# Performance work log

Measured on AMD Instinct MI355X. Metric: run time of the kernel, lower is better.

Reference implementation:

```python
import jax, jax.numpy as jnp
import numpy as np

N, E, F, H, R, NB, G, C = 100000, 500000, 128, 64, 16, 30, 1000, 10


def setup_inputs() -> dict:
    key = jax.random.key(0)
    ks = jax.random.split(key, 12)
    s = 0.05
    x = jax.random.normal(ks[0], (N, F), jnp.float32)
    edge_index = jax.random.randint(ks[1], (2, E), 0, N, dtype=jnp.int32)
    edge_norm = jax.random.uniform(ks[2], (E,), jnp.float32)
    edge_type = jax.random.randint(ks[3], (E,), 0, R, dtype=jnp.int32)
    seq_lengths = jnp.full((G,), N // G, dtype=jnp.int32)  # 1000 graphs x 100 nodes
    return dict(
        x=x, edge_index=edge_index, edge_norm=edge_norm, edge_type=edge_type,
        seq_lengths=seq_lengths, avec=0,
        w1_rel=jax.random.normal(ks[4], (F, H), jnp.float32) * s,
        w1_root=jax.random.normal(ks[5], (F, H), jnp.float32) * s,
        b1=jnp.zeros((H,), jnp.float32),
        bases=jax.random.normal(ks[6], (NB, H, H), jnp.float32) * s,
        comp=jax.random.normal(ks[7], (R, NB), jnp.float32) * s,
        w2_root=jax.random.normal(ks[8], (H, H), jnp.float32) * s,
        b2=jnp.zeros((H,), jnp.float32),
        lin_w=jax.random.normal(ks[9], (2 * (F + H), H), jnp.float32) * s,
        lin_b=jnp.zeros((H,), jnp.float32),
        fc_w=jax.random.normal(ks[10], (H, C), jnp.float32) * s,
        fc_b=jnp.zeros((C,), jnp.float32),
    )


def reference(x, edge_index, edge_norm, edge_type, seq_lengths, avec,
              w1_rel, w1_root, b1, bases, comp, w2_root, b2,
              lin_w, lin_b, fc_w, fc_b):
    src, dst = edge_index[0], edge_index[1]

    # --- GraphConv (PyG): out_i = W_rel @ sum_{j->i} w_ji x_j + W_root x_i + b
    msg = x[src] * edge_norm[:, None]                       # [E, F]
    agg = jax.ops.segment_sum(msg, dst, num_segments=N)     # [N, F]
    h = agg @ w1_rel + x @ w1_root + b1                     # [N, H]

    # --- RGCNConv with basis decomposition, mean aggregation per relation
    W = jnp.einsum('rb,bio->rio', comp, bases)              # [R, H, H]
    hs = h[src]                                             # [E, H]
    out = h @ w2_root + b2                                  # root transform + bias
    for r in range(R):  # small fixed relation count
        m = (edge_type == r).astype(h.dtype)                # [E]
        s_r = jax.ops.segment_sum(hs * m[:, None], dst, num_segments=N)
        c_r = jax.ops.segment_sum(m, dst, num_segments=N)
        out = out + (s_r / jnp.maximum(c_r, 1.0)[:, None]) @ W[r]

    feats = jnp.concatenate([x, out], axis=-1)              # [N, F+H]

    # --- ragged per-graph sum & max pooling (replaces the Python loop)
    bounds = jnp.cumsum(seq_lengths)
    gid = jnp.searchsorted(bounds, jnp.arange(N), side='right')  # [N] graph ids
    gsum = jax.ops.segment_sum(feats, gid, num_segments=G)       # [G, F+H]
    gmax = jax.ops.segment_max(feats, gid, num_segments=G)       # [G, F+H]

    hidden = jax.nn.relu(jnp.concatenate([gsum, gmax], -1) @ lin_w + lin_b)
    # dropout is identity at inference
    logits = hidden @ fc_w + fc_b                           # [G, C]
    if avec:
        return logits
    return jax.nn.log_softmax(logits, -1)
```

## Files before the change

kernel.cpp:

```cpp
#include <hip/hip_runtime.h>
#include <hip/hip_bf16.h>

#define NN 100000
#define NE 500000
#define FD 128
#define HD 64
#define RR 16
#define NBASE 30
#define GG 1000
#define CC 10
#define NGROUP 6250
#define NBLK ((NE + 255) / 256)
#define NDBLK ((NN + 256) / 256)
#define NOBLK (NN / 16)
#define TOTZ (NN * RR)
#define ZBLK ((TOTZ + 1023) / 1024)


typedef __attribute__((ext_vector_type(8))) short bf16x8;
typedef __attribute__((ext_vector_type(4))) float f32x4;

__device__ inline unsigned short f2b(float x) {
  __hip_bfloat16 b = __float2bfloat16(x);
  return *reinterpret_cast<unsigned short*>(&b);
}
__device__ inline float b2f(unsigned short u) {
  return __uint_as_float(((unsigned)u) << 16);
}
__device__ inline unsigned pk2(float a, float b) {
  return (unsigned)f2b(a) | ((unsigned)f2b(b) << 16);
}

__global__ void k_prep(const float* comp, const float* bases, const float* w_root,
                       const float* w_rel, const float* w2, unsigned short* Wt,
                       unsigned short* wcat2, unsigned short* w2t, int* zbase) {
  int bx = blockIdx.x;
  if (bx < 256) {
    int idx = bx * 256 + threadIdx.x;
    int r = idx >> 12, kj = idx & 4095;
    int k = kj >> 6, n = kj & 63;
    float acc = 0.0f;
    for (int b = 0; b < NBASE; ++b)
      acc += comp[r * NBASE + b] * bases[b * 4096 + kj];
    int sk = (k & 15) * 4 + (k >> 4);
    Wt[(r << 12) + n * 64 + sk] = f2b(acc);
  } else if (bx < 336) {
    int idx = (bx - 256) * 256 + threadIdx.x;
    if (idx < 16384) {
      int n = idx >> 7, k = idx & 127;
      float v = (n < 64) ? w_root[k * 64 + n] : w_rel[k * 64 + (n - 64)];
      int nt = n >> 4, m = n & 15;
      int s = k >> 5, q = (k >> 3) & 3, j = k & 7;
      wcat2[(((nt * 4 + s) * 64) + q * 16 + m) * 8 + j] = f2b(v);
    } else if (idx < 16384 + 4096) {
      int i2 = idx - 16384;
      int n = i2 >> 6, k = i2 & 63;
      int sk = (k & 15) * 4 + (k >> 4);
      w2t[n * 64 + sk] = f2b(w2[k * 64 + n]);
    }
  } else {
    int idx = (bx - 336) * 1024 + threadIdx.x * 4;
    if (idx < TOTZ)
      *reinterpret_cast<int4*>(zbase + idx) = make_int4(0, 0, 0, 0);
  }
}

__global__ __launch_bounds__(256) void k_proj_mfma(const float* x, const unsigned short* wcat2,
                                                   const float* b1, unsigned short* hroot_bf,
                                                   unsigned short* xw_bf) {
  __shared__ unsigned short wsh[16384];
  int wv = threadIdx.x >> 6, l = threadIdx.x & 63, m = l & 15, q = l >> 4;
  int g = blockIdx.x * 4 + wv;
  int gc = (g < NGROUP) ? g : (NGROUP - 1);
  size_t n0 = (size_t)gc * 16;
  const float* xr = x + (n0 + m) * FD + q * 8;
  float4 xv[8];
#pragma unroll
  for (int s = 0; s < 4; ++s) {
    xv[2 * s] = *reinterpret_cast<const float4*>(xr + s * 32);
    xv[2 * s + 1] = *reinterpret_cast<const float4*>(xr + s * 32 + 4);
  }
  {
    const uint4* wsrc = reinterpret_cast<const uint4*>(wcat2);
    uint4* wdst = reinterpret_cast<uint4*>(wsh);
#pragma unroll
    for (int r = 0; r < 8; ++r)
      wdst[r * 256 + threadIdx.x] = wsrc[r * 256 + threadIdx.x];
  }
  __syncthreads();
  if (g >= NGROUP) return;
  bf16x8 afr[4];
#pragma unroll
  for (int s = 0; s < 4; ++s) {
    float4 xa = xv[2 * s], xb = xv[2 * s + 1];
    bf16x8 a;
    a[0] = (short)f2b(xa.x); a[1] = (short)f2b(xa.y);
    a[2] = (short)f2b(xa.z); a[3] = (short)f2b(xa.w);
    a[4] = (short)f2b(xb.x); a[5] = (short)f2b(xb.y);
    a[6] = (short)f2b(xb.z); a[7] = (short)f2b(xb.w);
    afr[s] = a;
  }
  f32x4 acc[8];
#pragma unroll
  for (int nt = 0; nt < 8; ++nt) acc[nt] = (f32x4){0, 0, 0, 0};
#pragma unroll
  for (int s = 0; s < 4; ++s) {
#pragma unroll
    for (int nt = 0; nt < 8; ++nt) {
      bf16x8 b = *reinterpret_cast<const bf16x8*>(wsh + (size_t)((nt * 4 + s) * 64 + l) * 8);
      acc[nt] = __builtin_amdgcn_mfma_f32_16x16x32_bf16(afr[s], b, acc[nt], 0, 0, 0);
    }
  }
  float bv[4];
#pragma unroll
  for (int nt = 0; nt < 4; ++nt) bv[nt] = b1[nt * 16 + m];
#pragma unroll
  for (int i = 0; i < 4; ++i) {
    size_t row = (n0 + q * 4 + i) * 64 + m * 4;
    uint2 oh, ox;
    oh.x = pk2(acc[0][i] + bv[0], acc[1][i] + bv[1]);
    oh.y = pk2(acc[2][i] + bv[2], acc[3][i] + bv[3]);
    ox.x = pk2(acc[4][i], acc[5][i]);
    ox.y = pk2(acc[6][i], acc[7][i]);
    *reinterpret_cast<uint2*>(hroot_bf + row) = oh;
    *reinterpret_cast<uint2*>(xw_bf + row) = ox;
  }
}

__global__ void k_hists(const int* ei, const int* etype, int* bch, int* hist2) {
  __shared__ int lh[RR];
  if (threadIdx.x < RR) lh[threadIdx.x] = 0;
  __syncthreads();
  int e = blockIdx.x * 256 + threadIdx.x;
  if (e < NE) {
    int t = etype[e];
    atomicAdd(&lh[t], 1);
    atomicAdd(&hist2[ei[NE + e] * RR + t], 1);
  }
  __syncthreads();
  if (threadIdx.x < RR) bch[blockIdx.x * RR + threadIdx.x] = lh[threadIdx.x];
}

__device__ inline int block_scan_incl(int v, int* ps, int t) {
  ps[t] = v;
  __syncthreads();
  for (int off = 1; off < 256; off <<= 1) {
    int u = (t >= off) ? ps[t - off] : 0;
    __syncthreads();
    ps[t] += u;
    __syncthreads();
  }
  return ps[t];
}

__device__ inline int dst_degree(const int* hist2, int dst) {
  const int4* hp = reinterpret_cast<const int4*>(hist2 + dst * RR);
  int4 a = hp[0], b = hp[1], c = hp[2], d = hp[3];
  return a.x + a.y + a.z + a.w + b.x + b.y + b.z + b.w +
         c.x + c.y + c.z + c.w + d.x + d.y + d.z + d.w;
}

__global__ void k_scanA(const int* hist2, int* bsum) {
  __shared__ int red[256];
  int t = threadIdx.x;
  int dst = blockIdx.x * 256 + t;
  red[t] = (dst < NN) ? dst_degree(hist2, dst) : 0;
  __syncthreads();
  for (int s = 128; s; s >>= 1) {
    if (t < s) red[t] += red[t + s];
    __syncthreads();
  }
  if (t == 0) bsum[blockIdx.x] = red[0];
}

__global__ void k_scanC(const int* hist2, const int* bsum, int* rowptr_d, int* ctr_d) {
  int t = threadIdx.x;
  int dst = blockIdx.x * 256 + t;
  int v = (dst < NN) ? dst_degree(hist2, dst) : 0;
  __shared__ int ps[256];
  int incl = block_scan_incl(v, ps, t);
  int ex = bsum[blockIdx.x] + incl - v;
  if (dst <= NN) { rowptr_d[dst] = ex; ctr_d[dst] = ex; }
}

__global__ void k_bscan(const int* bch, const int* seq, int* bsum, int* bbase,
                        int* offs, int* bounds) {
  __shared__ int part[16][17], chunkbase[16][17];
  __shared__ int colbase[16];
  __shared__ int ps[256];
  int t = threadIdx.x;
  {
    int i0 = t * 2, i1 = t * 2 + 1;
    int l0 = (i0 < NDBLK) ? bsum[i0] : 0;
    int l1 = (i1 < NDBLK) ? bsum[i1] : 0;
    int sa = l0 + l1;
    int incla = block_scan_incl(sa, ps, t);
    int run = incla - sa;
    if (i0 < NDBLK) bsum[i0] = run;
    run += l0;
    if (i1 < NDBLK) bsum[i1] = run;
  }
  __syncthreads();
  int ty = t & 15, ck = t >> 4;
  const int CH = (NBLK + 15) / 16;
  int b0 = ck * CH, b1 = min(b0 + CH, NBLK);
  int s = 0;
  for (int b = b0; b < b1; ++b) s += bch[b * 16 + ty];
  part[ck][ty] = s;
  __syncthreads();
  if (t < 16) {
    int run = 0;
    for (int c = 0; c < 16; ++c) { chunkbase[c][t] = run; run += part[c][t]; }
    colbase[t] = run;
  }
  __syncthreads();
  if (t == 0) {
    int run = 0;
    for (int r = 0; r < RR; ++r) { int v = colbase[r]; offs[r] = run; colbase[r] = run; run += v; }
    offs[RR] = run;
  }
  __syncthreads();
  {
    int run = colbase[ty] + chunkbase[ck][ty];
    for (int b = b0; b < b1; ++b) {
      int v = bch[b * 16 + ty];
      bbase[b * 16 + ty] = run;
      run += v;
    }
  }
  __syncthreads();
  int loc[4];
  int ss = 0;
  if (t < 250) {
    for (int i = 0; i < 4; ++i) { loc[i] = seq[t * 4 + i]; ss += loc[i]; }
  }
  int incl = block_scan_incl(ss, ps, t);
  int base = incl - ss;
  if (t < 250) {
    int run = base;
    for (int i = 0; i < 4; ++i) { run += loc[i]; bounds[t * 4 + i] = run; }
  }
}

__global__ void k_sort(const int* ei, const int* etype, const float* enorm,
                       const int* bbase, const int* hist2, int* ctr_d,
                       uint4* tse, uint2* esen) {
  __shared__ int lcnt[RR];
  if (threadIdx.x < RR) lcnt[threadIdx.x] = 0;
  __syncthreads();
  int e = blockIdx.x * 256 + threadIdx.x;
  if (e >= NE) return;
  int t = etype[e];
  int rank = atomicAdd(&lcnt[t], 1);
  int p = bbase[blockIdx.x * RR + t] + rank;
  int src = ei[e];
  int dst = ei[NE + e];
  int cnt = hist2[dst * RR + t];
  float inv = 1.0f / (float)max(cnt, 1);
  int pos = atomicAdd(&ctr_d[dst], 1);
  esen[pos] = make_uint2((unsigned)src, __float_as_uint(enorm[e]));
  tse[p] = make_uint4((unsigned)src, __float_as_uint(inv), (unsigned)pos, 0u);
}

__global__ __launch_bounds__(256) void k_gconv_seg(const int* rowptr_d, const uint2* esen,
    const unsigned short* xw_bf, const unsigned short* hroot_bf, unsigned short* h_bf) {
  int wv = threadIdx.x >> 6, l = threadIdx.x & 63;
  int c4 = l & 15, eq = l >> 4;
  int dst = blockIdx.x * 4 + wv;
  int lo = rowptr_d[dst];
  int hi = rowptr_d[dst + 1];
  float4 acc = {0.0f, 0.0f, 0.0f, 0.0f};
  for (int base0 = lo; base0 < hi; base0 += 64) {
    int n = min(64, hi - base0);
    int sv = 0;
    float nv = 0.0f;
    if (l < n) {
      uint2 se = esen[base0 + l];
      sv = (int)se.x;
      nv = __uint_as_float(se.y);
    }
    int k4max = (n + 3) >> 2;
    for (int k4 = 0; k4 < k4max; ++k4) {
      int eid = k4 * 4 + eq;
      int s = __shfl(sv, eid);
      float w = __shfl(nv, eid);
      if (eid < n) {
        uint2 v = *reinterpret_cast<const uint2*>(xw_bf + (size_t)s * 64 + c4 * 4);
        acc.x += b2f((unsigned short)(v.x & 0xffffu)) * w;
        acc.y += b2f((unsigned short)(v.x >> 16)) * w;
        acc.z += b2f((unsigned short)(v.y & 0xffffu)) * w;
        acc.w += b2f((unsigned short)(v.y >> 16)) * w;
      }
    }
  }
  acc.x += __shfl_xor(acc.x, 16); acc.y += __shfl_xor(acc.y, 16);
  acc.z += __shfl_xor(acc.z, 16); acc.w += __shfl_xor(acc.w, 16);
  acc.x += __shfl_xor(acc.x, 32); acc.y += __shfl_xor(acc.y, 32);
  acc.z += __shfl_xor(acc.z, 32); acc.w += __shfl_xor(acc.w, 32);
  if (l < 16) {
    uint2 hb = *reinterpret_cast<const uint2*>(hroot_bf + (size_t)dst * 64 + l * 4);
    acc.x += b2f((unsigned short)(hb.x & 0xffffu));
    acc.y += b2f((unsigned short)(hb.x >> 16));
    acc.z += b2f((unsigned short)(hb.y & 0xffffu));
    acc.w += b2f((unsigned short)(hb.y >> 16));
    uint2 o;
    o.x = pk2(acc.x, acc.y);
    o.y = pk2(acc.z, acc.w);
    *reinterpret_cast<uint2*>(h_bf + (size_t)dst * 64 + l * 4) = o;
  }
}

__global__ __launch_bounds__(256) void k_rgcn_y(const uint4* tse, const int* offs,
    const unsigned short* h_bf, const unsigned short* Wt, unsigned short* y_bf) {
  int r = blockIdx.x;
  int lo = offs[r], hi = offs[r + 1];
  int cnt = hi - lo;
  int wv = threadIdx.x >> 6;
  int l = threadIdx.x & 63;
  int m = l & 15, q = l >> 4;
  int ngroups = (cnt + 15) / 16;
  const unsigned short* Wr = Wt + (r << 12);
  bf16x8 bfr[2][4];
#pragma unroll
  for (int s = 0; s < 2; ++s)
#pragma unroll
    for (int nt = 0; nt < 4; ++nt)
      bfr[s][nt] = *reinterpret_cast<const bf16x8*>(Wr + (nt * 16 + m) * 64 + s * 32 + q * 8);

  for (int g = blockIdx.y * 4 + wv; g < ngroups; g += gridDim.y * 4) {
    int base = lo + g * 16;
    int ne = min(16, hi - base);
    int p = base + ((m < ne) ? m : 0);
    uint4 t4 = tse[p];
    int src = (int)t4.x;
    float inv = __uint_as_float(t4.y);
    int pos = (int)t4.z;
    f32x4 acc[4];
#pragma unroll
    for (int nt = 0; nt < 4; ++nt) acc[nt] = (f32x4){0, 0, 0, 0};
    const unsigned short* hrow = h_bf + (size_t)src * 64 + q * 8;
#pragma unroll
    for (int s = 0; s < 2; ++s) {
      bf16x8 afr = *reinterpret_cast<const bf16x8*>(hrow + s * 32);
#pragma unroll
      for (int nt = 0; nt < 4; ++nt)
        acc[nt] = __builtin_amdgcn_mfma_f32_16x16x32_bf16(afr, bfr[s][nt], acc[nt], 0, 0, 0);
    }
#pragma unroll
    for (int i = 0; i < 4; ++i) {
      int row = q * 4 + i;
      float ir = __shfl(inv, row);
      int pr = __shfl(pos, row);
      if (row < ne) {
        uint2 o;
        o.x = pk2(acc[0][i] * ir, acc[1][i] * ir);
        o.y = pk2(acc[2][i] * ir, acc[3][i] * ir);
        *reinterpret_cast<uint2*>(y_bf + (size_t)pr * 64 + m * 4) = o;
      }
    }
  }
}

__global__ __launch_bounds__(256) void k_out(const int* rowptr_d, const unsigned short* y_bf,
    const unsigned short* h_bf, const unsigned short* w2t, const float* b2,
    const int* bounds, float* psum_p, float* pmax_p) {
  __shared__ float ldsC[16][68];
  __shared__ int gidv[16];
  int wv = threadIdx.x >> 6, l = threadIdx.x & 63;
  int c8 = l & 7, eq8 = l >> 3;
  size_t d0 = (size_t)blockIdx.x * 16;
  if (threadIdx.x < 16) {
    int dst = (int)d0 + threadIdx.x;
    int lo2 = 0, hi2 = GG;
    while (lo2 < hi2) {
      int mid = (lo2 + hi2) >> 1;
      if (bounds[mid] <= dst) lo2 = mid + 1; else hi2 = mid;
    }
    gidv[threadIdx.x] = lo2;
  }
  for (int dd = 0; dd < 4; ++dd) {
    int dst = (int)d0 + wv * 4 + dd;
    int lo = rowptr_d[dst];
    int hi = rowptr_d[dst + 1];
    float4 aA = {0.0f, 0.0f, 0.0f, 0.0f};
    float4 aB = {0.0f, 0.0f, 0.0f, 0.0f};
    for (int row = lo + eq8; row < hi; row += 8) {
      uint4 v = *reinterpret_cast<const uint4*>(y_bf + (size_t)row * 64 + c8 * 8);
      aA.x += b2f((unsigned short)(v.x & 0xffffu));
      aA.y += b2f((unsigned short)(v.x >> 16));
      aA.z += b2f((unsigned short)(v.y & 0xffffu));
      aA.w += b2f((unsigned short)(v.y >> 16));
      aB.x += b2f((unsigned short)(v.z & 0xffffu));
      aB.y += b2f((unsigned short)(v.z >> 16));
      aB.z += b2f((unsigned short)(v.w & 0xffffu));
      aB.w += b2f((unsigned short)(v.w >> 16));
    }
#pragma unroll
    for (int off = 8; off <= 32; off <<= 1) {
      aA.x += __shfl_xor(aA.x, off); aA.y += __shfl_xor(aA.y, off);
      aA.z += __shfl_xor(aA.z, off); aA.w += __shfl_xor(aA.w, off);
      aB.x += __shfl_xor(aB.x, off); aB.y += __shfl_xor(aB.y, off);
      aB.z += __shfl_xor(aB.z, off); aB.w += __shfl_xor(aB.w, off);
    }
    if (l < 8) {
      *reinterpret_cast<float4*>(&ldsC[wv * 4 + dd][l * 8]) = aA;
      *reinterpret_cast<float4*>(&ldsC[wv * 4 + dd][l * 8 + 4]) = aB;
    }
  }
  __syncthreads();
  int m = l & 15, q = l >> 4, nt = wv;
  float bb = b2[nt * 16 + m];
  f32x4 acc;
#pragma unroll
  for (int i = 0; i < 4; ++i) acc[i] = ldsC[q * 4 + i][m * 4 + nt] + bb;
#pragma unroll
  for (int s = 0; s < 2; ++s) {
    bf16x8 a = *reinterpret_cast<const bf16x8*>(h_bf + (d0 + m) * 64 + s * 32 + q * 8);
    bf16x8 b = *reinterpret_cast<const bf16x8*>(w2t + (nt * 16 + m) * 64 + s * 32 + q * 8);
    acc = __builtin_amdgcn_mfma_f32_16x16x32_bf16(a, b, acc, 0, 0, 0);
  }
  int c = nt * 16 + m;
  int gA = gidv[0];
  float sA = 0.0f, xA = -3.4e38f, sB = 0.0f, xB = -3.4e38f;
#pragma unroll
  for (int i = 0; i < 4; ++i) {
    int gi = gidv[q * 4 + i];
    if (gi == gA) { sA += acc[i]; xA = fmaxf(xA, acc[i]); }
    else          { sB += acc[i]; xB = fmaxf(xB, acc[i]); }
  }
#pragma unroll
  for (int off = 16; off <= 32; off <<= 1) {
    sA += __shfl_xor(sA, off); xA = fmaxf(xA, __shfl_xor(xA, off));
    sB += __shfl_xor(sB, off); xB = fmaxf(xB, __shfl_xor(xB, off));
  }
  if (q == 0) {
    size_t base = (size_t)blockIdx.x * 128;
    psum_p[base + c] = sA;
    psum_p[base + 64 + c] = sB;
    pmax_p[base + c] = xA;
    pmax_p[base + 64 + c] = xB;
  }
}

__global__ __launch_bounds__(256) void k_head(const float* x, const int* bounds,
    const float* psum_p, const float* pmax_p, const float* lin_w, const float* lin_b,
    const float* fc_w, const float* fc_b, float* dout) {
  __shared__ float4 psum[8][32], pmax[8][32];
  __shared__ float gsum[192], gmax[192];
  __shared__ float part[4][64];
  __shared__ float hid[HD], lg[CC], mred[2];
  int g = blockIdx.x, t = threadIdx.x;
  int lo = (g == 0) ? 0 : bounds[g - 1];
  int hi = bounds[g];
  int nn = hi - lo;
  {
    int c4 = t & 31, ch = t >> 5;
    int a = lo + (nn * ch) / 8, b = lo + (nn * (ch + 1)) / 8;
    float4 s = {0, 0, 0, 0};
    float4 mx = {-3.4e38f, -3.4e38f, -3.4e38f, -3.4e38f};
    const float* bp = x + (size_t)a * FD + c4 * 4;
    int n = a;
    for (; n + 4 <= b; n += 4) {
      float4 v0 = *reinterpret_cast<const float4*>(bp);
      float4 v1 = *reinterpret_cast<const float4*>(bp + FD);
      float4 v2 = *reinterpret_cast<const float4*>(bp + 2 * FD);
      float4 v3 = *reinterpret_cast<const float4*>(bp + 3 * FD);
      bp += 4 * FD;
      s.x += v0.x + v1.x + v2.x + v3.x;
      s.y += v0.y + v1.y + v2.y + v3.y;
      s.z += v0.z + v1.z + v2.z + v3.z;
      s.w += v0.w + v1.w + v2.w + v3.w;
      mx.x = fmaxf(fmaxf(fmaxf(mx.x, v0.x), fmaxf(v1.x, v2.x)), v3.x);
      mx.y = fmaxf(fmaxf(fmaxf(mx.y, v0.y), fmaxf(v1.y, v2.y)), v3.y);
      mx.z = fmaxf(fmaxf(fmaxf(mx.z, v0.z), fmaxf(v1.z, v2.z)), v3.z);
      mx.w = fmaxf(fmaxf(fmaxf(mx.w, v0.w), fmaxf(v1.w, v2.w)), v3.w);
    }
    for (; n < b; ++n) {
      float4 v = *reinterpret_cast<const float4*>(bp);
      bp += FD;
      s.x += v.x; s.y += v.y; s.z += v.z; s.w += v.w;
      mx.x = fmaxf(mx.x, v.x); mx.y = fmaxf(mx.y, v.y);
      mx.z = fmaxf(mx.z, v.z); mx.w = fmaxf(mx.w, v.w);
    }
    psum[ch][c4] = s;
    pmax[ch][c4] = mx;
  }
  __syncthreads();
  if (t < 32) {
    float4 s = psum[0][t], m = pmax[0][t];
#pragma unroll
    for (int ch = 1; ch < 8; ++ch) {
      float4 ps = psum[ch][t], pm = pmax[ch][t];
      s.x += ps.x; s.y += ps.y; s.z += ps.z; s.w += ps.w;
      m.x = fmaxf(m.x, pm.x); m.y = fmaxf(m.y, pm.y);
      m.z = fmaxf(m.z, pm.z); m.w = fmaxf(m.w, pm.w);
    }
    gsum[t * 4 + 0] = s.x; gsum[t * 4 + 1] = s.y;
    gsum[t * 4 + 2] = s.z; gsum[t * 4 + 3] = s.w;
    gmax[t * 4 + 0] = m.x; gmax[t * 4 + 1] = m.y;
    gmax[t * 4 + 2] = m.z; gmax[t * 4 + 3] = m.w;
  } else if (t < 96) {
    int c = t - 32;
    int blo = lo >> 4, bhi = (hi - 1) >> 4;
    float s = 0.0f, mx = -3.4e38f;
    for (int b = blo; b <= bhi; ++b) {
      size_t base = (size_t)b * 128;
      if (b * 16 >= lo) {
        s += psum_p[base + c];
        mx = fmaxf(mx, pmax_p[base + c]);
      }
      if (b * 16 + 15 < hi) {
        s += psum_p[base + 64 + c];
        mx = fmaxf(mx, pmax_p[base + 64 + c]);
      }
    }
    gsum[128 + c] = s;
    gmax[128 + c] = mx;
  }
  __syncthreads();
  {
    int o = t & 63, pp = t >> 6;
    float a = 0.0f;
    int k0 = pp * 96;
    for (int k = k0; k < k0 + 96; ++k) {
      float gv = (k < 192) ? gsum[k] : gmax[k - 192];
      a += gv * lin_w[k * 64 + o];
    }
    part[pp][o] = a;
  }
  __syncthreads();
  if (t < HD) {
    float a = lin_b[t] + part[0][t] + part[1][t] + part[2][t] + part[3][t];
    hid[t] = fmaxf(a, 0.0f);
  }
  __syncthreads();
  if (t < CC) {
    float a = fc_b[t];
    for (int k = 0; k < HD; ++k) a += hid[k] * fc_w[k * CC + t];
    lg[t] = a;
  }
  __syncthreads();
  if (t == 0) {
    float mm = lg[0];
#pragma unroll
    for (int i = 1; i < CC; ++i) mm = fmaxf(mm, lg[i]);
    float se = 0.0f;
#pragma unroll
    for (int i = 0; i < CC; ++i) se += __expf(lg[i] - mm);
    mred[0] = mm;
    mred[1] = __logf(se);
  }
  __syncthreads();
  if (t < CC) dout[g * CC + t] = lg[t] - mred[0] - mred[1];
}

extern "C" void kernel_launch(void* const* d_in, const int* in_sizes, int n_in,
                              void* d_out, int out_size, void* d_ws, size_t ws_size,
                              hipStream_t stream) {
  const float* x     = (const float*)d_in[0];
  const int* ei      = (const int*)d_in[1];
  const float* enorm = (const float*)d_in[2];
  const int* etype   = (const int*)d_in[3];
  const int* seq     = (const int*)d_in[4];
  const float* w1_rel  = (const float*)d_in[6];
  const float* w1_root = (const float*)d_in[7];
  const float* b1      = (const float*)d_in[8];
  const float* bases   = (const float*)d_in[9];
  const float* comp    = (const float*)d_in[10];
  const float* w2      = (const float*)d_in[11];
  const float* b2      = (const float*)d_in[12];
  const float* lin_w   = (const float*)d_in[13];
  const float* lin_b   = (const float*)d_in[14];
  const float* fc_w    = (const float*)d_in[15];
  const float* fc_b    = (const float*)d_in[16];
  float* dout = (float*)d_out;

  char* p = (char*)d_ws;
  unsigned short* hroot_bf = (unsigned short*)p; p += (size_t)NN * 64 * 2;
  unsigned short* xw_bf    = (unsigned short*)p; p += (size_t)NN * 64 * 2;
  unsigned short* y_bf = (unsigned short*)p; p += (size_t)NE * 64 * 2;
  unsigned short* h_bf = (unsigned short*)p; p += (size_t)NN * 64 * 2;
  unsigned short* Wt   = (unsigned short*)p; p += (size_t)RR * 4096 * 2;
  unsigned short* wcat2 = (unsigned short*)p; p += (size_t)128 * 128 * 2;
  unsigned short* w2t  = (unsigned short*)p; p += (size_t)64 * 64 * 2;
  uint4* tse   = (uint4*)p; p += (size_t)NE * 16;
  uint2* esen  = (uint2*)p; p += (size_t)NE * 8;
  int* hist2   = (int*)p; p += (size_t)NN * RR * 4;
  float* psum_p = (float*)p; p += (size_t)NOBLK * 128 * 4;
  float* pmax_p = (float*)p; p += (size_t)NOBLK * 128 * 4;
  int* rowptr_d = (int*)p; p += (size_t)(NDBLK * 256) * 4;
  int* ctr_d   = (int*)p; p += (size_t)(NDBLK * 256) * 4;
  int* bch     = (int*)p; p += (size_t)NBLK * RR * 4;
  int* bbase   = (int*)p; p += (size_t)NBLK * RR * 4;
  int* bsum    = (int*)p; p += (size_t)NGROUP * 4;
  int* offs    = (int*)p; p += 68;
  int* bounds  = (int*)p; p += (size_t)GG * 4;

  hipLaunchKernelGGL(k_prep, dim3(336 + ZBLK), dim3(256), 0, stream,
                     comp, bases, w1_root, w1_rel, w2, Wt, wcat2, w2t, hist2);
  hipLaunchKernelGGL(k_proj_mfma, dim3((NGROUP + 3) / 4), dim3(256), 0, stream,
                     x, wcat2, b1, hroot_bf, xw_bf);
  hipLaunchKernelGGL(k_hists, dim3(NBLK), dim3(256), 0, stream, ei, etype, bch, hist2);
  hipLaunchKernelGGL(k_scanA, dim3(NDBLK), dim3(256), 0, stream, hist2, bsum);
  hipLaunchKernelGGL(k_bscan, dim3(1), dim3(256), 0, stream, bch, seq, bsum, bbase, offs, bounds);
  hipLaunchKernelGGL(k_scanC, dim3(NDBLK), dim3(256), 0, stream, hist2, bsum, rowptr_d, ctr_d);
  hipLaunchKernelGGL(k_sort, dim3(NBLK), dim3(256), 0, stream,
                     ei, etype, enorm, bbase, hist2, ctr_d, tse, esen);
  hipLaunchKernelGGL(k_gconv_seg, dim3(NN / 4), dim3(256), 0, stream,
                     rowptr_d, esen, xw_bf, hroot_bf, h_bf);
  hipLaunchKernelGGL(k_rgcn_y, dim3(RR, 128), dim3(256), 0, stream,
                     tse, offs, h_bf, Wt, y_bf);
  hipLaunchKernelGGL(k_out, dim3(NOBLK), dim3(256), 0, stream,
                     rowptr_d, y_bf, h_bf, w2t, b2, bounds, psum_p, pmax_p);
  hipLaunchKernelGGL(k_head, dim3(GG), dim3(256), 0, stream, x, bounds,
                     psum_p, pmax_p, lin_w, lin_b, fc_w, fc_b, dout);
}
```

Before: 338.4 us.

## Fuse x pooling partials into projection kernel and narrow k_out gather lanes

```diff
diff --git a/kernel.cpp b/kernel.cpp
--- a/kernel.cpp
+++ b/kernel.cpp
@@ -13,6 +13,7 @@
 #define NBLK ((NE + 255) / 256)
 #define NDBLK ((NN + 256) / 256)
 #define NOBLK (NN / 16)
+#define NPBLK ((NGROUP + 3) / 4)
 #define TOTZ (NN * RR)
 #define ZBLK ((TOTZ + 1023) / 1024)
 
@@ -31,9 +32,22 @@
   return (unsigned)f2b(a) | ((unsigned)f2b(b) << 16);
 }
 
+__device__ inline int block_scan_incl(int v, int* ps, int t) {
+  ps[t] = v;
+  __syncthreads();
+  for (int off = 1; off < 256; off <<= 1) {
+    int u = (t >= off) ? ps[t - off] : 0;
+    __syncthreads();
+    ps[t] += u;
+    __syncthreads();
+  }
+  return ps[t];
+}
+
 __global__ void k_prep(const float* comp, const float* bases, const float* w_root,
-                       const float* w_rel, const float* w2, unsigned short* Wt,
-                       unsigned short* wcat2, unsigned short* w2t, int* zbase) {
+                       const float* w_rel, const float* w2, const int* seq,
+                       unsigned short* Wt, unsigned short* wcat2, unsigned short* w2t,
+                       int* zbase, int* bounds) {
   int bx = blockIdx.x;
   if (bx < 256) {
     int idx = bx * 256 + threadIdx.x;
@@ -58,20 +72,38 @@
       int sk = (k & 15) * 4 + (k >> 4);
       w2t[n * 64 + sk] = f2b(w2[k * 64 + n]);
     }
+  } else if (bx == 336) {
+    __shared__ int ps[256];
+    int t = threadIdx.x;
+    int loc[4];
+    int ss = 0;
+    if (t < 250) {
+      for (int i = 0; i < 4; ++i) { loc[i] = seq[t * 4 + i]; ss += loc[i]; }
+    }
+    int incl = block_scan_incl(ss, ps, t);
+    int base = incl - ss;
+    if (t < 250) {
+      int run = base;
+      for (int i = 0; i < 4; ++i) { run += loc[i]; bounds[t * 4 + i] = run; }
+    }
   } else {
-    int idx = (bx - 336) * 1024 + threadIdx.x * 4;
+    int idx = (bx - 337) * 1024 + threadIdx.x * 4;
     if (idx < TOTZ)
       *reinterpret_cast<int4*>(zbase + idx) = make_int4(0, 0, 0, 0);
   }
 }
 
 __global__ __launch_bounds__(256) void k_proj_mfma(const float* x, const unsigned short* wcat2,
-                                                   const float* b1, unsigned short* hroot_bf,
-                                                   unsigned short* xw_bf) {
+                                                   const float* b1, const int* bounds,
+                                                   unsigned short* hroot_bf, unsigned short* xw_bf,
+                                                   float* pxsum, float* pxmax) {
   __shared__ unsigned short wsh[16384];
+  __shared__ float pxs[4][2][128], pxm[4][2][128];
+  __shared__ int binfo;
   int wv = threadIdx.x >> 6, l = threadIdx.x & 63, m = l & 15, q = l >> 4;
   int g = blockIdx.x * 4 + wv;
-  int gc = (g < NGROUP) ? g : (NGROUP - 1);
+  bool active = (g < NGROUP);
+  int gc = active ? g : (NGROUP - 1);
   size_t n0 = (size_t)gc * 16;
   const float* xr = x + (n0 + m) * FD + q * 8;
   float4 xv[8];
@@ -87,8 +119,17 @@
     for (int r = 0; r < 8; ++r)
       wdst[r * 256 + threadIdx.x] = wsrc[r * 256 + threadIdx.x];
   }
-  __syncthreads();
-  if (g >= NGROUP) return;
+  if (threadIdx.x == 0) {
+    int n0b = blockIdx.x * 64;
+    int lo2 = 0, hi2 = GG;
+    while (lo2 < hi2) {
+      int mid = (lo2 + hi2) >> 1;
+      if (bounds[mid] <= n0b) lo2 = mid + 1; else hi2 = mid;
+    }
+    binfo = bounds[lo2];
+  }
+  __syncthreads();
+  int bnd = binfo;
   bf16x8 afr[4];
 #pragma unroll
   for (int s = 0; s < 4; ++s) {
@@ -111,19 +152,67 @@
       acc[nt] = __builtin_amdgcn_mfma_f32_16x16x32_bf16(afr[s], b, acc[nt], 0, 0, 0);
     }
   }
-  float bv[4];
-#pragma unroll
-  for (int nt = 0; nt < 4; ++nt) bv[nt] = b1[nt * 16 + m];
-#pragma unroll
-  for (int i = 0; i < 4; ++i) {
-    size_t row = (n0 + q * 4 + i) * 64 + m * 4;
-    uint2 oh, ox;
-    oh.x = pk2(acc[0][i] + bv[0], acc[1][i] + bv[1]);
-    oh.y = pk2(acc[2][i] + bv[2], acc[3][i] + bv[3]);
-    ox.x = pk2(acc[4][i], acc[5][i]);
-    ox.y = pk2(acc[6][i], acc[7][i]);
-    *reinterpret_cast<uint2*>(hroot_bf + row) = oh;
-    *reinterpret_cast<uint2*>(xw_bf + row) = ox;
+  if (active) {
+    float bv[4];
+#pragma unroll
+    for (int nt = 0; nt < 4; ++nt) bv[nt] = b1[nt * 16 + m];
+#pragma unroll
+    for (int i = 0; i < 4; ++i) {
+      size_t row = (n0 + q * 4 + i) * 64 + m * 4;
+      uint2 oh, ox;
+      oh.x = pk2(acc[0][i] + bv[0], acc[1][i] + bv[1]);
+      oh.y = pk2(acc[2][i] + bv[2], acc[3][i] + bv[3]);
+      ox.x = pk2(acc[4][i], acc[5][i]);
+      ox.y = pk2(acc[6][i], acc[7][i]);
+      *reinterpret_cast<uint2*>(hroot_bf + row) = oh;
+      *reinterpret_cast<uint2*>(xw_bf + row) = ox;
+    }
+  }
+  {
+    int row = (int)n0 + m;
+    bool inA = active && (row < bnd);
+    bool inB = active && (row >= bnd);
+#pragma unroll
+    for (int s = 0; s < 4; ++s) {
+      float v[8] = { xv[2 * s].x, xv[2 * s].y, xv[2 * s].z, xv[2 * s].w,
+                     xv[2 * s + 1].x, xv[2 * s + 1].y, xv[2 * s + 1].z, xv[2 * s + 1].w };
+#pragma unroll
+      for (int sl = 0; sl < 2; ++sl) {
+        bool in = sl ? inB : inA;
+        float sv[8], mv[8];
+#pragma unroll
+        for (int j = 0; j < 8; ++j) {
+          sv[j] = in ? v[j] : 0.0f;
+          mv[j] = in ? v[j] : -3.4e38f;
+        }
+#pragma unroll
+        for (int off = 1; off <= 8; off <<= 1) {
+#pragma unroll
+          for (int j = 0; j < 8; ++j) {
+            sv[j] += __shfl_xor(sv[j], off);
+            mv[j] = fmaxf(mv[j], __shfl_xor(mv[j], off));
+          }
+        }
+        if (m == 0) {
+#pragma unroll
+          for (int j = 0; j < 8; ++j) {
+            pxs[wv][sl][s * 32 + q * 8 + j] = sv[j];
+            pxm[wv][sl][s * 32 + q * 8 + j] = mv[j];
+          }
+        }
+      }
+    }
+  }
+  __syncthreads();
+  {
+    int t = threadIdx.x;
+    int sl = t >> 7, c = t & 127;
+    float s4 = pxs[0][sl][c] + pxs[1][sl][c] + pxs[2][sl][c] + pxs[3][sl][c];
+    float m4 = fmaxf(fmaxf(pxm[0][sl][c], pxm[1][sl][c]),
+                     fmaxf(pxm[2][sl][c], pxm[3][sl][c]));
+    size_t base = (size_t)blockIdx.x * 256 + sl * 128 + c;
+    pxsum[base] = s4;
+    pxmax[base] = m4;
   }
 }
 
@@ -139,18 +228,6 @@
   }
   __syncthreads();
   if (threadIdx.x < RR) bch[blockIdx.x * RR + threadIdx.x] = lh[threadIdx.x];
-}
-
-__device__ inline int block_scan_incl(int v, int* ps, int t) {
-  ps[t] = v;
-  __syncthreads();
-  for (int off = 1; off < 256; off <<= 1) {
-    int u = (t >= off) ? ps[t - off] : 0;
-    __syncthreads();
-    ps[t] += u;
-    __syncthreads();
-  }
-  return ps[t];
 }
 
 __device__ inline int dst_degree(const int* hist2, int dst) {
@@ -183,8 +260,7 @@
   if (dst <= NN) { rowptr_d[dst] = ex; ctr_d[dst] = ex; }
 }
 
-__global__ void k_bscan(const int* bch, const int* seq, int* bsum, int* bbase,
-                        int* offs, int* bounds) {
+__global__ void k_bscan(const int* bch, int* bsum, int* bbase, int* offs) {
   __shared__ int part[16][17], chunkbase[16][17];
   __shared__ int colbase[16];
   __shared__ int ps[256];
@@ -227,18 +303,6 @@
       bbase[b * 16 + ty] = run;
       run += v;
     }
-  }
-  __syncthreads();
-  int loc[4];
-  int ss = 0;
-  if (t < 250) {
-    for (int i = 0; i < 4; ++i) { loc[i] = seq[t * 4 + i]; ss += loc[i]; }
-  }
-  int incl = block_scan_incl(ss, ps, t);
-  int base = incl - ss;
-  if (t < 250) {
-    int run = base;
-    for (int i = 0; i < 4; ++i) { run += loc[i]; bounds[t * 4 + i] = run; }
   }
 }
 
@@ -367,7 +431,7 @@
   __shared__ float ldsC[16][68];
   __shared__ int gidv[16];
   int wv = threadIdx.x >> 6, l = threadIdx.x & 63;
-  int c8 = l & 7, eq8 = l >> 3;
+  int c4 = l & 15, eq = l >> 4;
   size_t d0 = (size_t)blockIdx.x * 16;
   if (threadIdx.x < 16) {
     int dst = (int)d0 + threadIdx.x;
@@ -382,30 +446,20 @@
     int dst = (int)d0 + wv * 4 + dd;
     int lo = rowptr_d[dst];
     int hi = rowptr_d[dst + 1];
-    float4 aA = {0.0f, 0.0f, 0.0f, 0.0f};
-    float4 aB = {0.0f, 0.0f, 0.0f, 0.0f};
-    for (int row = lo + eq8; row < hi; row += 8) {
-      uint4 v = *reinterpret_cast<const uint4*>(y_bf + (size_t)row * 64 + c8 * 8);
-      aA.x += b2f((unsigned short)(v.x & 0xffffu));
-      aA.y += b2f((unsigned short)(v.x >> 16));
-      aA.z += b2f((unsigned short)(v.y & 0xffffu));
-      aA.w += b2f((unsigned short)(v.y >> 16));
-      aB.x += b2f((unsigned short)(v.z & 0xffffu));
-      aB.y += b2f((unsigned short)(v.z >> 16));
-      aB.z += b2f((unsigned short)(v.w & 0xffffu));
-      aB.w += b2f((unsigned short)(v.w >> 16));
-    }
-#pragma unroll
-    for (int off = 8; off <= 32; off <<= 1) {
-      aA.x += __shfl_xor(aA.x, off); aA.y += __shfl_xor(aA.y, off);
-      aA.z += __shfl_xor(aA.z, off); aA.w += __shfl_xor(aA.w, off);
-      aB.x += __shfl_xor(aB.x, off); aB.y += __shfl_xor(aB.y, off);
-      aB.z += __shfl_xor(aB.z, off); aB.w += __shfl_xor(aB.w, off);
-    }
-    if (l < 8) {
-      *reinterpret_cast<float4*>(&ldsC[wv * 4 + dd][l * 8]) = aA;
-      *reinterpret_cast<float4*>(&ldsC[wv * 4 + dd][l * 8 + 4]) = aB;
-    }
+    float4 acc = {0.0f, 0.0f, 0.0f, 0.0f};
+    for (int row = lo + eq; row < hi; row += 4) {
+      uint2 v = *reinterpret_cast<const uint2*>(y_bf + (size_t)row * 64 + c4 * 4);
+      acc.x += b2f((unsigned short)(v.x & 0xffffu));
+      acc.y += b2f((unsigned short)(v.x >> 16));
+      acc.z += b2f((unsigned short)(v.y & 0xffffu));
+      acc.w += b2f((unsigned short)(v.y >> 16));
+    }
+    acc.x += __shfl_xor(acc.x, 16); acc.y += __shfl_xor(acc.y, 16);
+    acc.z += __shfl_xor(acc.z, 16); acc.w += __shfl_xor(acc.w, 16);
+    acc.x += __shfl_xor(acc.x, 32); acc.y += __shfl_xor(acc.y, 32);
+    acc.z += __shfl_xor(acc.z, 32); acc.w += __shfl_xor(acc.w, 32);
+    if (l < 16)
+      *reinterpret_cast<float4*>(&ldsC[wv * 4 + dd][l * 4]) = acc;
   }
   __syncthreads();
   int m = l & 15, q = l >> 4, nt = wv;
@@ -442,65 +496,35 @@
   }
 }
 
-__global__ __launch_bounds__(256) void k_head(const float* x, const int* bounds,
-    const float* psum_p, const float* pmax_p, const float* lin_w, const float* lin_b,
-    const float* fc_w, const float* fc_b, float* dout) {
-  __shared__ float4 psum[8][32], pmax[8][32];
+__global__ __launch_bounds__(256) void k_head(const int* bounds,
+    const float* pxsum, const float* pxmax, const float* psum_p, const float* pmax_p,
+    const float* lin_w, const float* lin_b, const float* fc_w, const float* fc_b,
+    float* dout) {
   __shared__ float gsum[192], gmax[192];
   __shared__ float part[4][64];
   __shared__ float hid[HD], lg[CC], mred[2];
   int g = blockIdx.x, t = threadIdx.x;
   int lo = (g == 0) ? 0 : bounds[g - 1];
   int hi = bounds[g];
-  int nn = hi - lo;
-  {
-    int c4 = t & 31, ch = t >> 5;
-    int a = lo + (nn * ch) / 8, b = lo + (nn * (ch + 1)) / 8;
-    float4 s = {0, 0, 0, 0};
-    float4 mx = {-3.4e38f, -3.4e38f, -3.4e38f, -3.4e38f};
-    const float* bp = x + (size_t)a * FD + c4 * 4;
-    int n = a;
-    for (; n + 4 <= b; n += 4) {
-      float4 v0 = *reinterpret_cast<const float4*>(bp);
-      float4 v1 = *reinterpret_cast<const float4*>(bp + FD);
-      float4 v2 = *reinterpret_cast<const float4*>(bp + 2 * FD);
-      float4 v3 = *reinterpret_cast<const float4*>(bp + 3 * FD);
-      bp += 4 * FD;
-      s.x += v0.x + v1.x + v2.x + v3.x;
-      s.y += v0.y + v1.y + v2.y + v3.y;
-      s.z += v0.z + v1.z + v2.z + v3.z;
-      s.w += v0.w + v1.w + v2.w + v3.w;
-      mx.x = fmaxf(fmaxf(fmaxf(mx.x, v0.x), fmaxf(v1.x, v2.x)), v3.x);
-      mx.y = fmaxf(fmaxf(fmaxf(mx.y, v0.y), fmaxf(v1.y, v2.y)), v3.y);
-      mx.z = fmaxf(fmaxf(fmaxf(mx.z, v0.z), fmaxf(v1.z, v2.z)), v3.z);
-      mx.w = fmaxf(fmaxf(fmaxf(mx.w, v0.w), fmaxf(v1.w, v2.w)), v3.w);
-    }
-    for (; n < b; ++n) {
-      float4 v = *reinterpret_cast<const float4*>(bp);
-      bp += FD;
-      s.x += v.x; s.y += v.y; s.z += v.z; s.w += v.w;
-      mx.x = fmaxf(mx.x, v.x); mx.y = fmaxf(mx.y, v.y);
-      mx.z = fmaxf(mx.z, v.z); mx.w = fmaxf(mx.w, v.w);
-    }
-    psum[ch][c4] = s;
-    pmax[ch][c4] = mx;
-  }
-  __syncthreads();
-  if (t < 32) {
-    float4 s = psum[0][t], m = pmax[0][t];
-#pragma unroll
-    for (int ch = 1; ch < 8; ++ch) {
-      float4 ps = psum[ch][t], pm = pmax[ch][t];
-      s.x += ps.x; s.y += ps.y; s.z += ps.z; s.w += ps.w;
-      m.x = fmaxf(m.x, pm.x); m.y = fmaxf(m.y, pm.y);
-      m.z = fmaxf(m.z, pm.z); m.w = fmaxf(m.w, pm.w);
-    }
-    gsum[t * 4 + 0] = s.x; gsum[t * 4 + 1] = s.y;
-    gsum[t * 4 + 2] = s.z; gsum[t * 4 + 3] = s.w;
-    gmax[t * 4 + 0] = m.x; gmax[t * 4 + 1] = m.y;
-    gmax[t * 4 + 2] = m.z; gmax[t * 4 + 3] = m.w;
-  } else if (t < 96) {
-    int c = t - 32;
+  if (t < 128) {
+    int c = t;
+    int blo = lo >> 6, bhi = (hi - 1) >> 6;
+    float s = 0.0f, mx = -3.4e38f;
+    for (int b = blo; b <= bhi; ++b) {
+      size_t base = (size_t)b * 256;
+      if (b * 64 >= lo) {
+        s += pxsum[base + c];
+        mx = fmaxf(mx, pxmax[base + c]);
+      }
+      if (b * 64 + 63 < hi) {
+        s += pxsum[base + 128 + c];
+        mx = fmaxf(mx, pxmax[base + 128 + c]);
+      }
+    }
+    gsum[c] = s;
+    gmax[c] = mx;
+  } else if (t < 192) {
+    int c = t - 128;
     int blo = lo >> 4, bhi = (hi - 1) >> 4;
     float s = 0.0f, mx = -3.4e38f;
     for (int b = blo; b <= bhi; ++b) {
@@ -588,6 +612,8 @@
   int* hist2   = (int*)p; p += (size_t)NN * RR * 4;
   float* psum_p = (float*)p; p += (size_t)NOBLK * 128 * 4;
   float* pmax_p = (float*)p; p += (size_t)NOBLK * 128 * 4;
+  float* pxsum = (float*)p; p += (size_t)NPBLK * 256 * 4;
+  float* pxmax = (float*)p; p += (size_t)NPBLK * 256 * 4;
   int* rowptr_d = (int*)p; p += (size_t)(NDBLK * 256) * 4;
   int* ctr_d   = (int*)p; p += (size_t)(NDBLK * 256) * 4;
   int* bch     = (int*)p; p += (size_t)NBLK * RR * 4;
@@ -596,13 +622,13 @@
   int* offs    = (int*)p; p += 68;
   int* bounds  = (int*)p; p += (size_t)GG * 4;
 
-  hipLaunchKernelGGL(k_prep, dim3(336 + ZBLK), dim3(256), 0, stream,
-                     comp, bases, w1_root, w1_rel, w2, Wt, wcat2, w2t, hist2);
-  hipLaunchKernelGGL(k_proj_mfma, dim3((NGROUP + 3) / 4), dim3(256), 0, stream,
-                     x, wcat2, b1, hroot_bf, xw_bf);
+  hipLaunchKernelGGL(k_prep, dim3(337 + ZBLK), dim3(256), 0, stream,
+                     comp, bases, w1_root, w1_rel, w2, seq, Wt, wcat2, w2t, hist2, bounds);
+  hipLaunchKernelGGL(k_proj_mfma, dim3(NPBLK), dim3(256), 0, stream,
+                     x, wcat2, b1, bounds, hroot_bf, xw_bf, pxsum, pxmax);
   hipLaunchKernelGGL(k_hists, dim3(NBLK), dim3(256), 0, stream, ei, etype, bch, hist2);
   hipLaunchKernelGGL(k_scanA, dim3(NDBLK), dim3(256), 0, stream, hist2, bsum);
-  hipLaunchKernelGGL(k_bscan, dim3(1), dim3(256), 0, stream, bch, seq, bsum, bbase, offs, bounds);
+  hipLaunchKernelGGL(k_bscan, dim3(1), dim3(256), 0, stream, bch, bsum, bbase, offs);
   hipLaunchKernelGGL(k_scanC, dim3(NDBLK), dim3(256), 0, stream, hist2, bsum, rowptr_d, ctr_d);
   hipLaunchKernelGGL(k_sort, dim3(NBLK), dim3(256), 0, stream,
                      ei, etype, enorm, bbase, hist2, ctr_d, tse, esen);
@@ -612,6 +638,6 @@
                      tse, offs, h_bf, Wt, y_bf);
   hipLaunchKernelGGL(k_out, dim3(NOBLK), dim3(256), 0, stream,
                      rowptr_d, y_bf, h_bf, w2t, b2, bounds, psum_p, pmax_p);
-  hipLaunchKernelGGL(k_head, dim3(GG), dim3(256), 0, stream, x, bounds,
-                     psum_p, pmax_p, lin_w, lin_b, fc_w, fc_b, dout);
-}
+  hipLaunchKernelGGL(k_head, dim3(GG), dim3(256), 0, stream, bounds,
+                     pxsum, pxmax, psum_p, pmax_p, lin_w, lin_b, fc_w, fc_b, dout);
+}
```

Result: slower. 364.1 us (+7.6%).
